# Kernel tuning notes

Hardware: AMD Instinct MI355X
Metric: run time of the kernel (lower is better)

Reference implementation:

```python
import jax, jax.numpy as jnp
import numpy as np

N_NODES = 50000
N_EDGES = 800000
HID = 256
MAX_ID = 10000

def _gcn(x, w, b, src, dst, ew, n):
    # PyG GCNConv with self-loops (weight 1.0): out = D^-1/2 (A+I) D^-1/2 (x W) + b
    xw = x @ w                                                   # [N, out]
    deg = jax.ops.segment_sum(ew, dst, num_segments=n) + 1.0     # self-loop adds 1
    dinv = jax.lax.rsqrt(deg)                                    # [N]
    norm = dinv[src] * ew * dinv[dst]                            # [E]
    agg = jax.ops.segment_sum(norm[:, None] * xw[src], dst, num_segments=n)
    agg = agg + (dinv * dinv)[:, None] * xw                      # self-loop term
    return agg + b

def setup_inputs() -> dict:
    key = jax.random.key(0)
    ks = jax.random.split(key, 24)
    s = 0.05
    inp = {
        "node_features": jax.random.normal(ks[0], (N_NODES, 3), jnp.float32),
        "edge_index": jax.random.randint(ks[1], (2, N_EDGES), 0, N_NODES),
        "edge_ids": jax.random.randint(ks[2], (N_EDGES,), 0, MAX_ID + 1),
        "edge_pos": jax.random.randint(ks[3], (N_EDGES,), 0, 3),
        "id_embed": jax.random.normal(ks[4], (MAX_ID + 1, 8), jnp.float32) * s,
        "pos_embed": jax.random.normal(ks[5], (3, 2), jnp.float32) * s,
        "ew_w1": jax.random.normal(ks[6], (10, 10), jnp.float32) * s,
        "ew_b1": jnp.zeros((10,), jnp.float32),
        "ew_w2": jax.random.normal(ks[7], (10, 1), jnp.float32) * s,
        "ew_b2": jnp.zeros((1,), jnp.float32),
        "conv1_w": jax.random.normal(ks[8], (3, HID), jnp.float32) * s,
        "conv1_b": jnp.zeros((HID,), jnp.float32),
        "conv2_w": jax.random.normal(ks[9], (HID, HID), jnp.float32) * s,
        "conv2_b": jnp.zeros((HID,), jnp.float32),
        "actor_w1": jax.random.normal(ks[10], (2 * HID, HID), jnp.float32) * s,
        "actor_b1": jnp.zeros((HID,), jnp.float32),
        "actor_w2": jax.random.normal(ks[11], (HID, 1), jnp.float32) * s,
        "actor_b2": jnp.zeros((1,), jnp.float32),
        "critic_w1": jax.random.normal(ks[12], (2 * HID, 2 * HID), jnp.float32) * s,
        "critic_b1": jnp.zeros((2 * HID,), jnp.float32),
        "critic_w2": jax.random.normal(ks[13], (2 * HID, HID), jnp.float32) * s,
        "critic_b2": jnp.zeros((HID,), jnp.float32),
        "critic_w3": jax.random.normal(ks[14], (HID, 1), jnp.float32) * s,
        "critic_b3": jnp.zeros((1,), jnp.float32),
    }
    return inp

def reference(node_features, edge_index, edge_ids, edge_pos, id_embed, pos_embed,
              ew_w1, ew_b1, ew_w2, ew_b2, conv1_w, conv1_b, conv2_w, conv2_b,
              actor_w1, actor_b1, actor_w2, actor_b2,
              critic_w1, critic_b1, critic_w2, critic_b2, critic_w3, critic_b3):
    n = node_features.shape[0]
    src, dst = edge_index[0], edge_index[1]
    # edge weight MLP: Linear-ReLU-Linear-Sigmoid on [id_embed(8) | pos_embed(2)]
    feat = jnp.concatenate([id_embed[edge_ids], pos_embed[edge_pos]], axis=1)  # [E,10]
    h = jax.nn.relu(feat @ ew_w1 + ew_b1)
    ew = jax.nn.sigmoid(h @ ew_w2 + ew_b2)[:, 0]                               # [E]
    # two GCN layers with ReLU
    x = jax.nn.relu(_gcn(node_features, conv1_w, conv1_b, src, dst, ew, n))
    x = jax.nn.relu(_gcn(x, conv2_w, conv2_b, src, dst, ew, n))
    # global mean pooling + concat
    g = jnp.mean(x, axis=0)                                                    # [H]
    combined = jnp.concatenate([x, jnp.broadcast_to(g, (n, g.shape[0]))], axis=1)
    # actor head
    a = jax.nn.relu(combined @ actor_w1 + actor_b1)
    action_logits = (a @ actor_w2 + actor_b2)[:, 0]                            # [N]
    # critic head on pooled features
    pooled = jnp.mean(combined, axis=0)[None, :]                               # [1,2H]
    c = jax.nn.relu(pooled @ critic_w1 + critic_b1)
    c = jax.nn.relu(c @ critic_w2 + critic_b2)
    state_value = (c @ critic_w3 + critic_b3)[0, 0]                            # scalar
    return action_logits, state_value
```

## Files before the change

### kernel.cpp

```cpp
#include <hip/hip_runtime.h>
#include <math.h>

#define HID 256

typedef __attribute__((ext_vector_type(8))) short short8;
typedef __attribute__((ext_vector_type(4))) float floatx4;

__device__ __forceinline__ ushort bf16_rne(float x) {
    uint u = __float_as_uint(x);
    uint r = (u + 0x7FFFu + ((u >> 16) & 1u)) >> 16;
    return (ushort)r;
}
__device__ __forceinline__ float bf16_to_f(ushort h) {
    return __uint_as_float(((uint)h) << 16);
}

__global__ void k_edge(const int* __restrict__ eid, const int* __restrict__ epos,
                       const float* __restrict__ id_emb, const float* __restrict__ pos_emb,
                       const float* __restrict__ w1, const float* __restrict__ b1,
                       const float* __restrict__ w2, const float* __restrict__ b2,
                       const int* __restrict__ ei, float* __restrict__ ew,
                       float* __restrict__ deg, int* __restrict__ cnt, int E) {
    __shared__ float sW1[100];
    __shared__ float sB1[10];
    __shared__ float sW2[10];
    __shared__ float sB2;
    int t = threadIdx.x;
    if (t < 100) sW1[t] = w1[t];
    if (t < 10) { sB1[t] = b1[t]; sW2[t] = w2[t]; }
    if (t == 0) sB2 = b2[0];
    __syncthreads();
    int e = blockIdx.x * blockDim.x + t;
    if (e >= E) return;
    int id = eid[e];
    int p  = epos[e];
    const float4* ide = (const float4*)(id_emb + (size_t)id * 8);
    float4 fa = ide[0], fb = ide[1];
    float f[10];
    f[0] = fa.x; f[1] = fa.y; f[2] = fa.z; f[3] = fa.w;
    f[4] = fb.x; f[5] = fb.y; f[6] = fb.z; f[7] = fb.w;
    f[8] = pos_emb[p * 2 + 0];
    f[9] = pos_emb[p * 2 + 1];
    float acc = sB2;
#pragma unroll
    for (int j = 0; j < 10; j++) {
        float h = sB1[j];
#pragma unroll
        for (int i = 0; i < 10; i++) h += f[i] * sW1[i * 10 + j];
        h = fmaxf(h, 0.f);
        acc += h * sW2[j];
    }
    float w = 1.f / (1.f + expf(-acc));
    ew[e] = w;
    int dst = ei[E + e];
    atomicAdd(&deg[dst], w);
    atomicAdd(&cnt[dst], 1);
}

__global__ void k_scan_a(const int* __restrict__ cnt, int* __restrict__ row_ptr,
                         int* __restrict__ bsums,
                         float* __restrict__ deg, const float* __restrict__ nf,
                         float4* __restrict__ nf4, float* __restrict__ gsum,
                         const float* __restrict__ w2, const float* __restrict__ aw1,
                         ushort* __restrict__ w2h, ushort* __restrict__ w2l,
                         ushort* __restrict__ a1h, ushort* __restrict__ a1l, int N) {
    __shared__ int s[256];
    int b = blockIdx.x, t = threadIdx.x;
    int i = b * 256 + t;
    if (b == 0) gsum[t] = 0.f;
    if (b < 64) {
        int gid = b * 256 + t;
        int mat = gid >> 13;
        int rem = gid & 8191;
        int c = rem >> 10;
        int tt = (rem >> 6) & 15;
        int L = rem & 63;
        int k0 = 32 * c + (L >> 4) * 8;
        int n  = 16 * tt + (L & 15);
        const float* W = mat ? aw1 : w2;
        ushort* H  = mat ? a1h : w2h;
        ushort* Lo = mat ? a1l : w2l;
        short8 hv, lv;
#pragma unroll
        for (int j = 0; j < 8; j++) {
            float x = W[(size_t)(k0 + j) * HID + n];
            ushort h = bf16_rne(x);
            hv[j] = (short)h;
            lv[j] = (short)bf16_rne(x - bf16_to_f(h));
        }
        size_t off = (size_t)rem * 8;
        *(short8*)(H + off) = hv;
        *(short8*)(Lo + off) = lv;
    }
    if (i < N) {
        deg[i] = 1.f / sqrtf(deg[i] + 1.f);
        nf4[i] = make_float4(nf[i * 3 + 0], nf[i * 3 + 1], nf[i * 3 + 2], 0.f);
    }
    int v = (i < N) ? cnt[i] : 0;
    s[t] = v;
    __syncthreads();
    for (int off = 1; off < 256; off <<= 1) {
        int u = (t >= off) ? s[t - off] : 0;
        __syncthreads();
        s[t] += u;
        __syncthreads();
    }
    int incl = s[t];
    if (i < N) row_ptr[i] = incl - v;
    if (t == 255) bsums[b] = incl;
}

__global__ void k_scan_c(int* __restrict__ row_ptr, int* __restrict__ cursor,
                         const int* __restrict__ bsums, int N, int NB) {
    __shared__ int s[256];
    int b = blockIdx.x, t = threadIdx.x;
    int v = (t < NB) ? bsums[t] : 0;
    s[t] = (t < b) ? v : 0;
    __syncthreads();
    for (int off = 128; off > 0; off >>= 1) {
        if (t < off) s[t] += s[t + off];
        __syncthreads();
    }
    int boff = s[0];
    int i = b * 256 + t;
    if (i < N) {
        int rp = row_ptr[i] + boff;
        row_ptr[i] = rp;
        cursor[i] = rp;
    }
    if (b == NB - 1) {
        __syncthreads();
        s[t] = (t < NB) ? bsums[t] : 0;
        __syncthreads();
        for (int off = 128; off > 0; off >>= 1) {
            if (t < off) s[t] += s[t + off];
            __syncthreads();
        }
        if (t == 0) row_ptr[N] = s[0];
    }
}

__global__ void k_fill(const int* __restrict__ ei, const float* __restrict__ ew,
                       const float* __restrict__ dinv, int* __restrict__ cursor,
                       int2* __restrict__ csr, int E) {
    int e = blockIdx.x * blockDim.x + threadIdx.x;
    if (e >= E) return;
    int src = ei[e];
    int dst = ei[E + e];
    int slot = atomicAdd(&cursor[dst], 1);
    float norm = dinv[src] * ew[e] * dinv[dst];
    csr[slot] = make_int2(src, __float_as_int(norm));
}

__global__ void k_agg3(const int* __restrict__ row_ptr, const int2* __restrict__ csr,
                       const float4* __restrict__ nf4, const float* __restrict__ dinv,
                       float4* __restrict__ T3, int N) {
    int n = blockIdx.x * blockDim.x + threadIdx.x;
    if (n >= N) return;
    int s = row_ptr[n];
    int e = row_ptr[n + 1];
    float ax = 0.f, ay = 0.f, az = 0.f;
    for (int i = s; i < e; i++) {
        int2 sn = csr[i];
        float w = __int_as_float(sn.y);
        float4 v = nf4[sn.x];
        ax = fmaf(w, v.x, ax);
        ay = fmaf(w, v.y, ay);
        az = fmaf(w, v.z, az);
    }
    float d = dinv[n];
    float dd = d * d;
    float4 v = nf4[n];
    ax = fmaf(dd, v.x, ax);
    ay = fmaf(dd, v.y, ay);
    az = fmaf(dd, v.z, az);
    T3[n] = make_float4(ax, ay, az, 0.f);
}

__global__ void k_gatherfused(const int* __restrict__ row_ptr, const int2* __restrict__ csr,
                              const float4* __restrict__ T3, const float* __restrict__ dinv,
                              const float* __restrict__ cw, const float* __restrict__ cb,
                              ushort* __restrict__ Ah, ushort* __restrict__ Al, int N) {
    int lane = threadIdx.x & 63;
    int wv = threadIdx.x >> 6;
    int n = blockIdx.x * 4 + wv;
    if (n >= N) return;
    const float4 w0 = *(const float4*)(cw + 4 * lane);
    const float4 w1 = *(const float4*)(cw + HID + 4 * lane);
    const float4 w2 = *(const float4*)(cw + 2 * HID + 4 * lane);
    const float4 bv = *(const float4*)(cb + 4 * lane);
    int s = row_ptr[n];
    int e = row_ptr[n + 1];
    float4 acc = make_float4(0.f, 0.f, 0.f, 0.f);
    for (int i = s; i < e; i++) {
        int2 sn = csr[i];
        float w = __int_as_float(sn.y);
        float4 t = T3[sn.x];
        float xx = fmaxf(fmaf(t.x, w0.x, fmaf(t.y, w1.x, fmaf(t.z, w2.x, bv.x))), 0.f);
        float xy = fmaxf(fmaf(t.x, w0.y, fmaf(t.y, w1.y, fmaf(t.z, w2.y, bv.y))), 0.f);
        float xz = fmaxf(fmaf(t.x, w0.z, fmaf(t.y, w1.z, fmaf(t.z, w2.z, bv.z))), 0.f);
        float xw = fmaxf(fmaf(t.x, w0.w, fmaf(t.y, w1.w, fmaf(t.z, w2.w, bv.w))), 0.f);
        acc.x = fmaf(w, xx, acc.x);
        acc.y = fmaf(w, xy, acc.y);
        acc.z = fmaf(w, xz, acc.z);
        acc.w = fmaf(w, xw, acc.w);
    }
    float d = dinv[n];
    float dd = d * d;
    float4 t = T3[n];
    float xx = fmaxf(fmaf(t.x, w0.x, fmaf(t.y, w1.x, fmaf(t.z, w2.x, bv.x))), 0.f);
    float xy = fmaxf(fmaf(t.x, w0.y, fmaf(t.y, w1.y, fmaf(t.z, w2.y, bv.y))), 0.f);
    float xz = fmaxf(fmaf(t.x, w0.z, fmaf(t.y, w1.z, fmaf(t.z, w2.z, bv.z))), 0.f);
    float xw = fmaxf(fmaf(t.x, w0.w, fmaf(t.y, w1.w, fmaf(t.z, w2.w, bv.w))), 0.f);
    acc.x = fmaf(dd, xx, acc.x);
    acc.y = fmaf(dd, xy, acc.y);
    acc.z = fmaf(dd, xz, acc.z);
    acc.w = fmaf(dd, xw, acc.w);
    ushort4 hv, lv;
    ushort h;
    h = bf16_rne(acc.x); hv.x = h; lv.x = bf16_rne(acc.x - bf16_to_f(h));
    h = bf16_rne(acc.y); hv.y = h; lv.y = bf16_rne(acc.y - bf16_to_f(h));
    h = bf16_rne(acc.z); hv.z = h; lv.z = bf16_rne(acc.z - bf16_to_f(h));
    h = bf16_rne(acc.w); hv.w = h; lv.w = bf16_rne(acc.w - bf16_to_f(h));
    size_t base = (size_t)n * HID + lane * 4;
    *(ushort4*)(Ah + base) = hv;
    *(ushort4*)(Al + base) = lv;
}

#define ASTRIDE 264

__global__ __launch_bounds__(256, 2) void k_gemm_mfma(
        const ushort* __restrict__ Ah, const ushort* __restrict__ Al,
        const float* __restrict__ b2,
        const ushort* __restrict__ w2h, const ushort* __restrict__ w2l,
        const ushort* __restrict__ a1h, const ushort* __restrict__ a1l,
        float* __restrict__ P, float* __restrict__ gsum, int N) {
    __shared__ ushort Hs[64 * ASTRIDE];
    __shared__ ushort Ls[64 * ASTRIDE];
    int tid = threadIdx.x;
    int n0 = blockIdx.x * 64;
    int w = tid >> 6;
    int L = tid & 63;
    int quad = L >> 4, ln = L & 15;

    int arow[4];
#pragma unroll
    for (int mt = 0; mt < 4; mt++) {
        int r = n0 + mt * 16 + ln;
        arow[mt] = (r < N) ? r : (N - 1);
    }

    floatx4 acc[4][4];
#pragma unroll
    for (int i = 0; i < 4; i++)
#pragma unroll
        for (int j = 0; j < 4; j++) acc[i][j] = 0.f;

    for (int c = 0; c < 8; c++) {
        short8 ahf[4], alf[4];
#pragma unroll
        for (int mt = 0; mt < 4; mt++) {
            size_t ab = (size_t)arow[mt] * HID + 32 * c + quad * 8;
            ahf[mt] = *(const short8*)(Ah + ab);
            alf[mt] = *(const short8*)(Al + ab);
        }
#pragma unroll
        for (int nt = 0; nt < 4; nt++) {
            int t = 4 * w + nt;
            size_t off = ((size_t)(c * 16 + t) * 64 + L) * 8;
            short8 bh = *(const short8*)(w2h + off);
            short8 bl = *(const short8*)(w2l + off);
#pragma unroll
            for (int mt = 0; mt < 4; mt++) {
                acc[nt][mt] = __builtin_amdgcn_mfma_f32_16x16x32_bf16(ahf[mt], bh, acc[nt][mt], 0, 0, 0);
                acc[nt][mt] = __builtin_amdgcn_mfma_f32_16x16x32_bf16(ahf[mt], bl, acc[nt][mt], 0, 0, 0);
                acc[nt][mt] = __builtin_amdgcn_mfma_f32_16x16x32_bf16(alf[mt], bh, acc[nt][mt], 0, 0, 0);
            }
        }
    }

#pragma unroll
    for (int nt = 0; nt < 4; nt++) {
        int col = (4 * w + nt) * 16 + ln;
        float bb = b2[col];
        float s = 0.f;
#pragma unroll
        for (int mt = 0; mt < 4; mt++) {
#pragma unroll
            for (int r = 0; r < 4; r++) {
                int row = n0 + mt * 16 + quad * 4 + r;
                float v = fmaxf(acc[nt][mt][r] + bb, 0.f);
                acc[nt][mt][r] = v;
                if (row < N) s += v;
            }
        }
        s += __shfl_down(s, 32, 64);
        s += __shfl_down(s, 16, 64);
        if (L < 16) atomicAdd(&gsum[col], s);
    }

#pragma unroll
    for (int nt = 0; nt < 4; nt++) {
        int col = (4 * w + nt) * 16 + ln;
#pragma unroll
        for (int mt = 0; mt < 4; mt++) {
#pragma unroll
            for (int r = 0; r < 4; r++) {
                int row = mt * 16 + quad * 4 + r;
                float v = acc[nt][mt][r];
                ushort h = bf16_rne(v);
                Hs[row * ASTRIDE + col] = h;
                Ls[row * ASTRIDE + col] = bf16_rne(v - bf16_to_f(h));
            }
        }
    }
    __syncthreads();

    floatx4 acc2[4][4];
#pragma unroll
    for (int i = 0; i < 4; i++)
#pragma unroll
        for (int j = 0; j < 4; j++) acc2[i][j] = 0.f;

    for (int c = 0; c < 8; c++) {
        short8 ahf[4], alf[4];
#pragma unroll
        for (int mt = 0; mt < 4; mt++) {
            int base = (mt * 16 + ln) * ASTRIDE + 32 * c + quad * 8;
            ahf[mt] = *(const short8*)&Hs[base];
            alf[mt] = *(const short8*)&Ls[base];
        }
#pragma unroll
        for (int nt = 0; nt < 4; nt++) {
            int t = 4 * w + nt;
            size_t off = ((size_t)(c * 16 + t) * 64 + L) * 8;
            short8 bh = *(const short8*)(a1h + off);
            short8 bl = *(const short8*)(a1l + off);
#pragma unroll
            for (int mt = 0; mt < 4; mt++) {
                acc2[nt][mt] = __builtin_amdgcn_mfma_f32_16x16x32_bf16(ahf[mt], bh, acc2[nt][mt], 0, 0, 0);
                acc2[nt][mt] = __builtin_amdgcn_mfma_f32_16x16x32_bf16(ahf[mt], bl, acc2[nt][mt], 0, 0, 0);
                acc2[nt][mt] = __builtin_amdgcn_mfma_f32_16x16x32_bf16(alf[mt], bh, acc2[nt][mt], 0, 0, 0);
            }
        }
    }

#pragma unroll
    for (int nt = 0; nt < 4; nt++) {
        int col = (4 * w + nt) * 16 + ln;
#pragma unroll
        for (int mt = 0; mt < 4; mt++) {
#pragma unroll
            for (int r = 0; r < 4; r++) {
                int row = n0 + mt * 16 + quad * 4 + r;
                if (row < N) P[(size_t)row * HID + col] = acc2[nt][mt][r];
            }
        }
    }
}

__global__ void k_logits(const float* __restrict__ P, const float* __restrict__ gbias,
                         const float* __restrict__ aw2, const float* __restrict__ ab2,
                         float* __restrict__ out, int N) {
    int lane = threadIdx.x & 63;
    int wv = threadIdx.x >> 6;
    int n = blockIdx.x * 4 + wv;
    if (n >= N) return;
    float4 p = *(const float4*)(P + (size_t)n * HID + 4 * lane);
    float4 gb = *(const float4*)(gbias + 4 * lane);
    float4 w2 = *(const float4*)(aw2 + 4 * lane);
    float v = fmaxf(p.x + gb.x, 0.f) * w2.x
            + fmaxf(p.y + gb.y, 0.f) * w2.y
            + fmaxf(p.z + gb.z, 0.f) * w2.z
            + fmaxf(p.w + gb.w, 0.f) * w2.w;
#pragma unroll
    for (int off = 32; off > 0; off >>= 1) v += __shfl_down(v, off, 64);
    if (lane == 0) out[n] = v + ab2[0];
}

__global__ void k_heads(const float* __restrict__ gsum,
                        const float* __restrict__ aw1, const float* __restrict__ ab1,
                        float* __restrict__ gbias,
                        const float* __restrict__ cw1, const float* __restrict__ cb1,
                        const float* __restrict__ cw2, const float* __restrict__ cb2,
                        const float* __restrict__ cw3, const float* __restrict__ cb3,
                        float* __restrict__ sv_out, float invN) {
    int t = threadIdx.x;
    if (blockIdx.x == 0) {
        if (t < HID) {
            float s = ab1[t];
            for (int j = 0; j < HID; j++) s += gsum[j] * invN * aw1[(HID + j) * HID + t];
            gbias[t] = s;
        }
        return;
    }
    __shared__ float p[2 * HID];
    __shared__ float c1[2 * HID];
    __shared__ float c2[HID];
    p[t] = gsum[t & (HID - 1)] * invN;
    __syncthreads();
    float s = cb1[t];
    for (int i = 0; i < 2 * HID; i++) s += p[i] * cw1[i * 2 * HID + t];
    c1[t] = fmaxf(s, 0.f);
    __syncthreads();
    if (t < HID) {
        float s2 = cb2[t];
        for (int i = 0; i < 2 * HID; i++) s2 += c1[i] * cw2[i * HID + t];
        c2[t] = fmaxf(s2, 0.f) * cw3[t];
    }
    __syncthreads();
    for (int st = HID / 2; st > 0; st >>= 1) {
        if (t < st) c2[t] += c2[t + st];
        __syncthreads();
    }
    if (t == 0) sv_out[0] = c2[0] + cb3[0];
}

extern "C" void kernel_launch(void* const* d_in, const int* in_sizes, int n_in,
                              void* d_out, int out_size, void* d_ws, size_t ws_size,
                              hipStream_t stream) {
    const float* nf      = (const float*)d_in[0];
    const int*   ei      = (const int*)d_in[1];
    const int*   eid     = (const int*)d_in[2];
    const int*   epos    = (const int*)d_in[3];
    const float* id_emb  = (const float*)d_in[4];
    const float* pos_emb = (const float*)d_in[5];
    const float* ew_w1   = (const float*)d_in[6];
    const float* ew_b1   = (const float*)d_in[7];
    const float* ew_w2   = (const float*)d_in[8];
    const float* ew_b2   = (const float*)d_in[9];
    const float* c1w     = (const float*)d_in[10];
    const float* c1b     = (const float*)d_in[11];
    const float* c2w     = (const float*)d_in[12];
    const float* c2b     = (const float*)d_in[13];
    const float* aw1     = (const float*)d_in[14];
    const float* ab1     = (const float*)d_in[15];
    const float* aw2     = (const float*)d_in[16];
    const float* ab2     = (const float*)d_in[17];
    const float* cw1     = (const float*)d_in[18];
    const float* cb1     = (const float*)d_in[19];
    const float* cw2     = (const float*)d_in[20];
    const float* cb2     = (const float*)d_in[21];
    const float* cw3     = (const float*)d_in[22];
    const float* cb3     = (const float*)d_in[23];

    int N = in_sizes[0] / 3;
    int E = in_sizes[2];
    int NB = (N + 255) / 256;
    float invN = 1.f / (float)N;

    char* ws = (char*)d_ws;
    float* deg      = (float*)ws;                         ws += (size_t)N * 4;
    int*   cnt      = (int*)ws;                           ws += (size_t)N * 4;
    float* gsum     = (float*)ws;                         ws += HID * 4;
    ushort* Ah      = (ushort*)ws;                        ws += (size_t)N * HID * 2;
    ushort* Al      = (ushort*)ws;                        ws += (size_t)N * HID * 2;
    float* P        = (float*)ws;                         ws += (size_t)N * HID * 4;
    float* ew       = (float*)ws;                         ws += (size_t)E * 4;
    int2*  csr      = (int2*)ws;                          ws += (size_t)E * 8;
    int*   row_ptr  = (int*)ws;                           ws += (size_t)(N + 1) * 4;
    int*   cursor   = (int*)ws;                           ws += (size_t)N * 4;
    int*   bsums    = (int*)ws;                           ws += 256 * 4;
    float4* T3      = (float4*)ws;                        ws += (size_t)N * 16;
    float4* nf4     = (float4*)ws;                        ws += (size_t)N * 16;
    float* gbias    = (float*)ws;                         ws += HID * 4;
    ushort* w2h     = (ushort*)ws;                        ws += 65536 * 2;
    ushort* w2l     = (ushort*)ws;                        ws += 65536 * 2;
    ushort* a1h     = (ushort*)ws;                        ws += 65536 * 2;
    ushort* a1l     = (ushort*)ws;                        ws += 65536 * 2;

    float* out = (float*)d_out;

    hipMemsetAsync(deg, 0, (size_t)(2 * N) * sizeof(float), stream);

    k_edge<<<(E + 255) / 256, 256, 0, stream>>>(eid, epos, id_emb, pos_emb,
                                                ew_w1, ew_b1, ew_w2, ew_b2, ei, ew, deg, cnt, E);

    k_scan_a<<<NB, 256, 0, stream>>>(cnt, row_ptr, bsums, deg, nf, nf4, gsum,
                                     c2w, aw1, w2h, w2l, a1h, a1l, N);
    k_scan_c<<<NB, 256, 0, stream>>>(row_ptr, cursor, bsums, N, NB);

    k_fill<<<(E + 255) / 256, 256, 0, stream>>>(ei, ew, deg, cursor, csr, E);

    k_agg3<<<(N + 255) / 256, 256, 0, stream>>>(row_ptr, csr, nf4, deg, T3, N);

    k_gatherfused<<<(N + 3) / 4, 256, 0, stream>>>(row_ptr, csr, T3, deg, c1w, c1b, Ah, Al, N);

    k_gemm_mfma<<<(N + 63) / 64, 256, 0, stream>>>(Ah, Al, c2b, w2h, w2l, a1h, a1l, P, gsum, N);

    k_heads<<<2, 2 * HID, 0, stream>>>(gsum, aw1, ab1, gbias,
                                       cw1, cb1, cw2, cb2, cw3, cb3, out + N, invN);

    k_logits<<<(N + 3) / 4, 256, 0, stream>>>(P, gbias, aw2, ab2, out, N);
}
```

Baseline: 448.7 us.

## Split GEMM into two kernels, fuse heads via last-block ticket and logits epilogue

Splits the fused two-GEMM kernel into a conv2 GEMM, which writes the bf16 hi/lo activations to global memory, and an actor GEMM whose epilogue computes the logits directly. This removes the fp32 P buffer and the separate logits kernel. The head MLPs now run in the last block of the first GEMM, chosen by an atomic ticket, which removes the separate heads launch. Edge degree and count are packed into a single 64-bit fixed-point atomic, halving the atomics per edge at the cost of quantising edge weights to 2^-20. The trade-off is an extra global round trip for the activations and serial head work running on a single block.

```diff
diff --git a/kernel.cpp b/kernel.cpp
--- a/kernel.cpp
+++ b/kernel.cpp
@@ -20,7 +20,7 @@
                        const float* __restrict__ w1, const float* __restrict__ b1,
                        const float* __restrict__ w2, const float* __restrict__ b2,
                        const int* __restrict__ ei, float* __restrict__ ew,
-                       float* __restrict__ deg, int* __restrict__ cnt, int E) {
+                       unsigned long long* __restrict__ cnt64, int E) {
     __shared__ float sW1[100];
     __shared__ float sB1[10];
     __shared__ float sW2[10];
@@ -53,21 +53,20 @@
     float w = 1.f / (1.f + expf(-acc));
     ew[e] = w;
     int dst = ei[E + e];
-    atomicAdd(&deg[dst], w);
-    atomicAdd(&cnt[dst], 1);
-}
-
-__global__ void k_scan_a(const int* __restrict__ cnt, int* __restrict__ row_ptr,
-                         int* __restrict__ bsums,
+    unsigned long long pack = (1ull << 40) + (unsigned long long)(w * 1048576.0f + 0.5f);
+    atomicAdd(&cnt64[dst], pack);
+}
+
+__global__ void k_scan_a(const unsigned long long* __restrict__ cnt64,
+                         int* __restrict__ row_ptr, int* __restrict__ bsums,
                          float* __restrict__ deg, const float* __restrict__ nf,
-                         float4* __restrict__ nf4, float* __restrict__ gsum,
+                         float4* __restrict__ nf4,
                          const float* __restrict__ w2, const float* __restrict__ aw1,
                          ushort* __restrict__ w2h, ushort* __restrict__ w2l,
                          ushort* __restrict__ a1h, ushort* __restrict__ a1l, int N) {
     __shared__ int s[256];
     int b = blockIdx.x, t = threadIdx.x;
     int i = b * 256 + t;
-    if (b == 0) gsum[t] = 0.f;
     if (b < 64) {
         int gid = b * 256 + t;
         int mat = gid >> 13;
@@ -92,11 +91,14 @@
         *(short8*)(H + off) = hv;
         *(short8*)(Lo + off) = lv;
     }
+    int v = 0;
     if (i < N) {
-        deg[i] = 1.f / sqrtf(deg[i] + 1.f);
+        unsigned long long cv = cnt64[i];
+        v = (int)(cv >> 40);
+        float degf = (float)(cv & 0xFFFFFFFFFFull) * (1.0f / 1048576.0f);
+        deg[i] = 1.f / sqrtf(degf + 1.f);
         nf4[i] = make_float4(nf[i * 3 + 0], nf[i * 3 + 1], nf[i * 3 + 2], 0.f);
     }
-    int v = (i < N) ? cnt[i] : 0;
     s[t] = v;
     __syncthreads();
     for (int off = 1; off < 256; off <<= 1) {
@@ -227,16 +229,18 @@
     *(ushort4*)(Al + base) = lv;
 }
 
-#define ASTRIDE 264
-
-__global__ __launch_bounds__(256, 2) void k_gemm_mfma(
+__global__ __launch_bounds__(256) void k_gemm1(
         const ushort* __restrict__ Ah, const ushort* __restrict__ Al,
         const float* __restrict__ b2,
         const ushort* __restrict__ w2h, const ushort* __restrict__ w2l,
-        const ushort* __restrict__ a1h, const ushort* __restrict__ a1l,
-        float* __restrict__ P, float* __restrict__ gsum, int N) {
-    __shared__ ushort Hs[64 * ASTRIDE];
-    __shared__ ushort Ls[64 * ASTRIDE];
+        ushort* __restrict__ x2h, ushort* __restrict__ x2l,
+        float* __restrict__ gsum, int* __restrict__ ticket,
+        const float* __restrict__ aw1, const float* __restrict__ ab1,
+        float* __restrict__ gbias,
+        const float* __restrict__ cw1, const float* __restrict__ cb1,
+        const float* __restrict__ cw2, const float* __restrict__ cb2,
+        const float* __restrict__ cw3, const float* __restrict__ cb3,
+        float* __restrict__ sv_out, float invN, int N, int nblocks) {
     int tid = threadIdx.x;
     int n0 = blockIdx.x * 64;
     int w = tid >> 6;
@@ -291,7 +295,12 @@
                 int row = n0 + mt * 16 + quad * 4 + r;
                 float v = fmaxf(acc[nt][mt][r] + bb, 0.f);
                 acc[nt][mt][r] = v;
-                if (row < N) s += v;
+                if (row < N) {
+                    s += v;
+                    ushort h = bf16_rne(v);
+                    x2h[(size_t)row * HID + col] = h;
+                    x2l[(size_t)row * HID + col] = bf16_rne(v - bf16_to_f(h));
+                }
             }
         }
         s += __shfl_down(s, 32, 64);
@@ -299,36 +308,77 @@
         if (L < 16) atomicAdd(&gsum[col], s);
     }
 
-#pragma unroll
-    for (int nt = 0; nt < 4; nt++) {
-        int col = (4 * w + nt) * 16 + ln;
-#pragma unroll
-        for (int mt = 0; mt < 4; mt++) {
-#pragma unroll
-            for (int r = 0; r < 4; r++) {
-                int row = mt * 16 + quad * 4 + r;
-                float v = acc[nt][mt][r];
-                ushort h = bf16_rne(v);
-                Hs[row * ASTRIDE + col] = h;
-                Ls[row * ASTRIDE + col] = bf16_rne(v - bf16_to_f(h));
-            }
-        }
-    }
-    __syncthreads();
-
-    floatx4 acc2[4][4];
+    __threadfence();
+    __shared__ int amLast;
+    if (tid == 0) amLast = (atomicAdd(ticket, 1) == nblocks - 1) ? 1 : 0;
+    __syncthreads();
+    if (!amLast) return;
+
+    __shared__ float sg[HID];
+    sg[tid] = atomicAdd(&gsum[tid], 0.0f) * invN;
+    __syncthreads();
+    {
+        float s = ab1[tid];
+        for (int j = 0; j < HID; j++) s += sg[j] * aw1[(HID + j) * HID + tid];
+        gbias[tid] = s;
+    }
+    __shared__ float p[2 * HID];
+    __shared__ float c1[2 * HID];
+    __shared__ float c2[HID];
+    p[tid] = sg[tid];
+    p[tid + HID] = sg[tid];
+    __syncthreads();
+    for (int col = tid; col < 2 * HID; col += 256) {
+        float s = cb1[col];
+        for (int k = 0; k < 2 * HID; k++) s += p[k] * cw1[k * 2 * HID + col];
+        c1[col] = fmaxf(s, 0.f);
+    }
+    __syncthreads();
+    {
+        float s2 = cb2[tid];
+        for (int k = 0; k < 2 * HID; k++) s2 += c1[k] * cw2[k * HID + tid];
+        c2[tid] = fmaxf(s2, 0.f) * cw3[tid];
+    }
+    __syncthreads();
+    for (int st = 128; st > 0; st >>= 1) {
+        if (tid < st) c2[tid] += c2[tid + st];
+        __syncthreads();
+    }
+    if (tid == 0) sv_out[0] = c2[0] + cb3[0];
+}
+
+__global__ __launch_bounds__(256) void k_gemm2(
+        const ushort* __restrict__ x2h, const ushort* __restrict__ x2l,
+        const ushort* __restrict__ a1h, const ushort* __restrict__ a1l,
+        const float* __restrict__ gbias, const float* __restrict__ aw2,
+        const float* __restrict__ ab2, float* __restrict__ out, int N) {
+    __shared__ float red[64 * 4];
+    int tid = threadIdx.x;
+    int n0 = blockIdx.x * 64;
+    int w = tid >> 6;
+    int L = tid & 63;
+    int quad = L >> 4, ln = L & 15;
+
+    int arow[4];
+#pragma unroll
+    for (int mt = 0; mt < 4; mt++) {
+        int r = n0 + mt * 16 + ln;
+        arow[mt] = (r < N) ? r : (N - 1);
+    }
+
+    floatx4 acc[4][4];
 #pragma unroll
     for (int i = 0; i < 4; i++)
 #pragma unroll
-        for (int j = 0; j < 4; j++) acc2[i][j] = 0.f;
+        for (int j = 0; j < 4; j++) acc[i][j] = 0.f;
 
     for (int c = 0; c < 8; c++) {
         short8 ahf[4], alf[4];
 #pragma unroll
         for (int mt = 0; mt < 4; mt++) {
-            int base = (mt * 16 + ln) * ASTRIDE + 32 * c + quad * 8;
-            ahf[mt] = *(const short8*)&Hs[base];
-            alf[mt] = *(const short8*)&Ls[base];
+            size_t ab = (size_t)arow[mt] * HID + 32 * c + quad * 8;
+            ahf[mt] = *(const short8*)(x2h + ab);
+            alf[mt] = *(const short8*)(x2l + ab);
         }
 #pragma unroll
         for (int nt = 0; nt < 4; nt++) {
@@ -338,82 +388,43 @@
             short8 bl = *(const short8*)(a1l + off);
 #pragma unroll
             for (int mt = 0; mt < 4; mt++) {
-                acc2[nt][mt] = __builtin_amdgcn_mfma_f32_16x16x32_bf16(ahf[mt], bh, acc2[nt][mt], 0, 0, 0);
-                acc2[nt][mt] = __builtin_amdgcn_mfma_f32_16x16x32_bf16(ahf[mt], bl, acc2[nt][mt], 0, 0, 0);
-                acc2[nt][mt] = __builtin_amdgcn_mfma_f32_16x16x32_bf16(alf[mt], bh, acc2[nt][mt], 0, 0, 0);
+                acc[nt][mt] = __builtin_amdgcn_mfma_f32_16x16x32_bf16(ahf[mt], bh, acc[nt][mt], 0, 0, 0);
+                acc[nt][mt] = __builtin_amdgcn_mfma_f32_16x16x32_bf16(ahf[mt], bl, acc[nt][mt], 0, 0, 0);
+                acc[nt][mt] = __builtin_amdgcn_mfma_f32_16x16x32_bf16(alf[mt], bh, acc[nt][mt], 0, 0, 0);
             }
         }
     }
 
+    float gb[4], w2c[4];
 #pragma unroll
     for (int nt = 0; nt < 4; nt++) {
         int col = (4 * w + nt) * 16 + ln;
-#pragma unroll
-        for (int mt = 0; mt < 4; mt++) {
-#pragma unroll
-            for (int r = 0; r < 4; r++) {
-                int row = n0 + mt * 16 + quad * 4 + r;
-                if (row < N) P[(size_t)row * HID + col] = acc2[nt][mt][r];
-            }
-        }
-    }
-}
-
-__global__ void k_logits(const float* __restrict__ P, const float* __restrict__ gbias,
-                         const float* __restrict__ aw2, const float* __restrict__ ab2,
-                         float* __restrict__ out, int N) {
-    int lane = threadIdx.x & 63;
-    int wv = threadIdx.x >> 6;
-    int n = blockIdx.x * 4 + wv;
-    if (n >= N) return;
-    float4 p = *(const float4*)(P + (size_t)n * HID + 4 * lane);
-    float4 gb = *(const float4*)(gbias + 4 * lane);
-    float4 w2 = *(const float4*)(aw2 + 4 * lane);
-    float v = fmaxf(p.x + gb.x, 0.f) * w2.x
-            + fmaxf(p.y + gb.y, 0.f) * w2.y
-            + fmaxf(p.z + gb.z, 0.f) * w2.z
-            + fmaxf(p.w + gb.w, 0.f) * w2.w;
-#pragma unroll
-    for (int off = 32; off > 0; off >>= 1) v += __shfl_down(v, off, 64);
-    if (lane == 0) out[n] = v + ab2[0];
-}
-
-__global__ void k_heads(const float* __restrict__ gsum,
-                        const float* __restrict__ aw1, const float* __restrict__ ab1,
-                        float* __restrict__ gbias,
-                        const float* __restrict__ cw1, const float* __restrict__ cb1,
-                        const float* __restrict__ cw2, const float* __restrict__ cb2,
-                        const float* __restrict__ cw3, const float* __restrict__ cb3,
-                        float* __restrict__ sv_out, float invN) {
-    int t = threadIdx.x;
-    if (blockIdx.x == 0) {
-        if (t < HID) {
-            float s = ab1[t];
-            for (int j = 0; j < HID; j++) s += gsum[j] * invN * aw1[(HID + j) * HID + t];
-            gbias[t] = s;
-        }
-        return;
-    }
-    __shared__ float p[2 * HID];
-    __shared__ float c1[2 * HID];
-    __shared__ float c2[HID];
-    p[t] = gsum[t & (HID - 1)] * invN;
-    __syncthreads();
-    float s = cb1[t];
-    for (int i = 0; i < 2 * HID; i++) s += p[i] * cw1[i * 2 * HID + t];
-    c1[t] = fmaxf(s, 0.f);
-    __syncthreads();
-    if (t < HID) {
-        float s2 = cb2[t];
-        for (int i = 0; i < 2 * HID; i++) s2 += c1[i] * cw2[i * HID + t];
-        c2[t] = fmaxf(s2, 0.f) * cw3[t];
-    }
-    __syncthreads();
-    for (int st = HID / 2; st > 0; st >>= 1) {
-        if (t < st) c2[t] += c2[t + st];
-        __syncthreads();
-    }
-    if (t == 0) sv_out[0] = c2[0] + cb3[0];
+        gb[nt] = gbias[col];
+        w2c[nt] = aw2[col];
+    }
+#pragma unroll
+    for (int mt = 0; mt < 4; mt++) {
+#pragma unroll
+        for (int r = 0; r < 4; r++) {
+            float s = 0.f;
+#pragma unroll
+            for (int nt = 0; nt < 4; nt++)
+                s += fmaxf(acc[nt][mt][r] + gb[nt], 0.f) * w2c[nt];
+            s += __shfl_xor(s, 1, 64);
+            s += __shfl_xor(s, 2, 64);
+            s += __shfl_xor(s, 4, 64);
+            s += __shfl_xor(s, 8, 64);
+            int row = mt * 16 + quad * 4 + r;
+            if (ln == 0) red[row * 4 + w] = s;
+        }
+    }
+    __syncthreads();
+    if (tid < 64) {
+        int n = n0 + tid;
+        if (n < N)
+            out[n] = red[tid * 4 + 0] + red[tid * 4 + 1]
+                   + red[tid * 4 + 2] + red[tid * 4 + 3] + ab2[0];
+    }
 }
 
 extern "C" void kernel_launch(void* const* d_in, const int* in_sizes, int n_in,
@@ -447,15 +458,18 @@
     int N = in_sizes[0] / 3;
     int E = in_sizes[2];
     int NB = (N + 255) / 256;
+    int NG = (N + 63) / 64;
     float invN = 1.f / (float)N;
 
     char* ws = (char*)d_ws;
+    unsigned long long* cnt64 = (unsigned long long*)ws;  ws += (size_t)N * 8;
+    float* gsum     = (float*)ws;                         ws += HID * 4;
+    int*   ticket   = (int*)ws;                           ws += 2 * 4;
     float* deg      = (float*)ws;                         ws += (size_t)N * 4;
-    int*   cnt      = (int*)ws;                           ws += (size_t)N * 4;
-    float* gsum     = (float*)ws;                         ws += HID * 4;
     ushort* Ah      = (ushort*)ws;                        ws += (size_t)N * HID * 2;
     ushort* Al      = (ushort*)ws;                        ws += (size_t)N * HID * 2;
-    float* P        = (float*)ws;                         ws += (size_t)N * HID * 4;
+    ushort* x2h     = (ushort*)ws;                        ws += (size_t)N * HID * 2;
+    ushort* x2l     = (ushort*)ws;                        ws += (size_t)N * HID * 2;
     float* ew       = (float*)ws;                         ws += (size_t)E * 4;
     int2*  csr      = (int2*)ws;                          ws += (size_t)E * 8;
     int*   row_ptr  = (int*)ws;                           ws += (size_t)(N + 1) * 4;
@@ -471,12 +485,12 @@
 
     float* out = (float*)d_out;
 
-    hipMemsetAsync(deg, 0, (size_t)(2 * N) * sizeof(float), stream);
+    hipMemsetAsync(cnt64, 0, (size_t)N * 8 + HID * 4 + 8, stream);
 
     k_edge<<<(E + 255) / 256, 256, 0, stream>>>(eid, epos, id_emb, pos_emb,
-                                                ew_w1, ew_b1, ew_w2, ew_b2, ei, ew, deg, cnt, E);
-
-    k_scan_a<<<NB, 256, 0, stream>>>(cnt, row_ptr, bsums, deg, nf, nf4, gsum,
+                                                ew_w1, ew_b1, ew_w2, ew_b2, ei, ew, cnt64, E);
+
+    k_scan_a<<<NB, 256, 0, stream>>>(cnt64, row_ptr, bsums, deg, nf, nf4,
                                      c2w, aw1, w2h, w2l, a1h, a1l, N);
     k_scan_c<<<NB, 256, 0, stream>>>(row_ptr, cursor, bsums, N, NB);
 
@@ -486,10 +500,9 @@
 
     k_gatherfused<<<(N + 3) / 4, 256, 0, stream>>>(row_ptr, csr, T3, deg, c1w, c1b, Ah, Al, N);
 
-    k_gemm_mfma<<<(N + 63) / 64, 256, 0, stream>>>(Ah, Al, c2b, w2h, w2l, a1h, a1l, P, gsum, N);
-
-    k_heads<<<2, 2 * HID, 0, stream>>>(gsum, aw1, ab1, gbias,
-                                       cw1, cb1, cw2, cb2, cw3, cb3, out + N, invN);
-
-    k_logits<<<(N + 3) / 4, 256, 0, stream>>>(P, gbias, aw2, ab2, out, N);
-}
+    k_gemm1<<<NG, 256, 0, stream>>>(Ah, Al, c2b, w2h, w2l, x2h, x2l, gsum, ticket,
+                                    aw1, ab1, gbias, cw1, cb1, cw2, cb2, cw3, cb3,
+                                    out + N, invN, N, NG);
+
+    k_gemm2<<<NG, 256, 0, stream>>>(x2h, x2l, a1h, a1l, gbias, aw2, ab2, out, N);
+}
```

Result: slower. 568.1 us (+26.6%).
